# Performance work log

Measured on AMD Instinct MI355X. Metric: run time of the kernel, lower is better.

The kernel has to match this reference:

```python
import jax, jax.numpy as jnp
import numpy as np

B, S, I, H = 32, 512, 512, 512


def _lstm_dir(x_seq, Wih, Whh, bih, bhh, reverse):
    """Run a PyTorch-style LSTMCell over time. x_seq: [S, B, I]."""
    bsz = x_seq.shape[1]
    hid = Whh.shape[1]
    h0 = jnp.zeros((bsz, hid), x_seq.dtype)
    c0 = jnp.zeros((bsz, hid), x_seq.dtype)
    b = bih + bhh

    def step(carry, x_t):
        h, c = carry
        g = x_t @ Wih.T + h @ Whh.T + b           # [B, 4H]
        i_g, f_g, g_g, o_g = jnp.split(g, 4, axis=-1)
        c = jax.nn.sigmoid(f_g) * c + jax.nn.sigmoid(i_g) * jnp.tanh(g_g)
        h = jax.nn.sigmoid(o_g) * jnp.tanh(c)
        return (h, c), h

    (hN, cN), hs = jax.lax.scan(step, (h0, c0), x_seq, reverse=reverse)
    # with reverse=True, hs[t] is aligned with x_seq[t] (matches ht_b[::-1])
    return hs, hN, cN


def setup_inputs() -> dict:
    key = jax.random.key(0)
    ks = jax.random.split(key, 9)
    bound = 1.0 / np.sqrt(H)
    u = lambda k, shp: jax.random.uniform(k, shp, jnp.float32, -bound, bound)
    return {
        "X": jax.random.normal(ks[0], (B, S, I), jnp.float32),
        "Wih_f": u(ks[1], (4 * H, I)),
        "Whh_f": u(ks[2], (4 * H, H)),
        "bih_f": u(ks[3], (4 * H,)),
        "bhh_f": u(ks[4], (4 * H,)),
        "Wih_b": u(ks[5], (4 * H, I)),
        "Whh_b": u(ks[6], (4 * H, H)),
        "bih_b": u(ks[7], (4 * H,)),
        "bhh_b": u(ks[8], (4 * H,)),
    }


def reference(X, Wih_f, Whh_f, bih_f, bhh_f, Wih_b, Whh_b, bih_b, bhh_b):
    x_seq = jnp.transpose(X, (1, 0, 2))  # [S, B, I]
    hs_f, hN_f, cN_f = _lstm_dir(x_seq, Wih_f, Whh_f, bih_f, bhh_f, False)
    hs_b, hN_b, cN_b = _lstm_dir(x_seq, Wih_b, Whh_b, bih_b, bhh_b, True)
    # ht: [B, S, 2H]
    ht = jnp.transpose(jnp.concatenate([hs_f, hs_b], axis=-1), (1, 0, 2))
    stacked_h = jnp.stack([hN_f, hN_b])  # [2, B, H] (forward final, backward final)
    stacked_c = jnp.stack([cN_f, cN_b])
    return ht, (stacked_h, stacked_c)
```

## Files before the change

kernel.cpp:

```cpp
#include <hip/hip_runtime.h>
#include <hip/hip_bf16.h>

#define BSZ 32
#define SSZ 512
#define ISZ 512
#define HSZ 512
#define XB_OFF   0ull
#define HEX_OFF  (16ull << 20)
#define CTR_OFF  (HEX_OFF + (128ull << 10))

typedef __attribute__((ext_vector_type(8)))  short short8;
typedef __attribute__((ext_vector_type(4)))  float f32x4;
typedef __attribute__((ext_vector_type(4)))  unsigned short us4;
typedef __attribute__((ext_vector_type(4)))  int i32x4;

__device__ __forceinline__ unsigned short f2bf(float f) {
    union { float f; unsigned u; } v; v.f = f;
    unsigned r = v.u + 0x7fffu + ((v.u >> 16) & 1u);
    return (unsigned short)(r >> 16);
}

__device__ __forceinline__ float sigf(float x) { return 1.0f / (1.0f + __expf(-x)); }
__device__ __forceinline__ float tanhfast(float x) {
    float a = fabsf(x);
    float e = __expf(-2.0f * a);
    float t = (1.0f - e) / (1.0f + e);
    return x < 0.0f ? -t : t;
}

__global__ void k_xpose(const float* __restrict__ X, unsigned short* __restrict__ Xb) {
    int idx = blockIdx.x * 256 + threadIdx.x;
    int i4 = idx & 127;
    int t  = (idx >> 7) & 511;
    int b  = idx >> 16;
    float4 v = reinterpret_cast<const float4*>(X)[idx];
    us4 o = { f2bf(v.x), f2bf(v.y), f2bf(v.z), f2bf(v.w) };
    *reinterpret_cast<us4*>(Xb + (size_t)t * 16384 + (size_t)(i4 >> 1) * 256 + b * 8 + (i4 & 1) * 4) = o;
}

__launch_bounds__(256, 1)
__global__ void k_bilstm(const float* __restrict__ Wih_f, const float* __restrict__ Whh_f,
                         const float* __restrict__ bih_f, const float* __restrict__ bhh_f,
                         const float* __restrict__ Wih_b, const float* __restrict__ Whh_b,
                         const float* __restrict__ bih_b, const float* __restrict__ bhh_b,
                         const unsigned short* __restrict__ Xb,
                         unsigned short* h_ex, unsigned* flags, float* __restrict__ out)
{
    const int tid = threadIdx.x;
    const int grp = blockIdx.x & 7;
    if (grp >= 2) return;
    const int dir = grp;
    const int p   = blockIdx.x >> 3;
    const int wv  = tid >> 6;
    const int ln  = tid & 63;
    const int kh  = wv >> 1;
    const int sub = wv & 1;
    const int q   = ln >> 4;
    const int m15 = ln & 15;

    unsigned* tab = flags + 4096;
    {
        unsigned xcc;
        asm volatile("s_getreg_b32 %0, hwreg(20, 0, 32)" : "=s"(xcc));
        if (tid == 0)
            __hip_atomic_store(tab + dir * 32 + p, (xcc & 7u) + 1u,
                               __ATOMIC_RELAXED, __HIP_MEMORY_SCOPE_AGENT);
    }

    const float* Wih = dir ? Wih_b : Wih_f;
    const float* Whh = dir ? Whh_b : Whh_f;
    const float* bi  = dir ? bih_b : bih_f;
    const float* bh  = dir ? bhh_b : bhh_f;

    __shared__ float gates[3][32][67];
    __shared__ float cst[32][16];
    __shared__ float bias[64];
    __shared__ int   mode_sh;

    short8 breg[32];
    if (kh == 0) {
#pragma unroll
        for (int ks = 0; ks < 16; ++ks)
#pragma unroll
            for (int gg = 0; gg < 2; ++gg) {
                const float* wr = Wih + (size_t)((sub * 2 + gg) * 512 + p * 16 + m15) * 512
                                      + ks * 32 + q * 8;
                short8 bb;
#pragma unroll
                for (int j = 0; j < 8; ++j) bb[j] = (short)f2bf(wr[j]);
                breg[ks * 2 + gg] = bb;
            }
    } else {
#pragma unroll
        for (int ks = 0; ks < 8; ++ks)
#pragma unroll
            for (int g = 0; g < 4; ++g) {
                const float* wr = Whh + (size_t)(g * 512 + p * 16 + m15) * 512
                                      + sub * 256 + ks * 32 + q * 8;
                short8 bb;
#pragma unroll
                for (int j = 0; j < 8; ++j) bb[j] = (short)f2bf(wr[j]);
                breg[ks * 4 + g] = bb;
            }
    }

    if (tid < 64) {
        int c = tid;
        int gr = (c >> 4) * 512 + p * 16 + (c & 15);
        bias[c] = bi[gr] + bh[gr];
    }
    for (int i = tid; i < 512; i += 256) ((float*)cst)[i] = 0.0f;

    if (tid < 64) {
        const unsigned* tp = tab + dir * 32 + (tid & 31);
        unsigned v;
        do { v = __hip_atomic_load(tp, __ATOMIC_RELAXED, __HIP_MEMORY_SCOPE_AGENT); } while (v == 0u);
        unsigned ref = __shfl(v, 0);
        int same = (__ballot(v == ref) == ~0ull) ? 1 : 0;
        if (tid == 0) mode_sh = same;
    }
    __syncthreads();
    const int fast = mode_sh;

    unsigned* flg = flags + (size_t)dir * 2048;
    unsigned short* hexd = h_ex + (size_t)dir * 2 * 16384;

    int agent_poll = 0;

    for (int s = 0; s < 512; ++s) {
        const int t = dir ? (511 - s) : s;
        f32x4 acc[4][2];
#pragma unroll
        for (int g = 0; g < 4; ++g) { acc[g][0] = {0.f,0.f,0.f,0.f}; acc[g][1] = {0.f,0.f,0.f,0.f}; }

        if (kh == 0) {
            const unsigned short* abase = Xb + (size_t)t * 16384;
#pragma unroll
            for (int ks = 0; ks < 16; ++ks) {
                const unsigned short* ap = abase + (size_t)(ks * 4 + q) * 256 + m15 * 8;
                short8 a0 = *reinterpret_cast<const short8*>(ap);
                short8 a1 = *reinterpret_cast<const short8*>(ap + 128);
                acc[0][0] = __builtin_amdgcn_mfma_f32_16x16x32_bf16(a0, breg[ks * 2 + 0], acc[0][0], 0, 0, 0);
                acc[1][0] = __builtin_amdgcn_mfma_f32_16x16x32_bf16(a0, breg[ks * 2 + 1], acc[1][0], 0, 0, 0);
                acc[0][1] = __builtin_amdgcn_mfma_f32_16x16x32_bf16(a1, breg[ks * 2 + 0], acc[0][1], 0, 0, 0);
                acc[1][1] = __builtin_amdgcn_mfma_f32_16x16x32_bf16(a1, breg[ks * 2 + 1], acc[1][1], 0, 0, 0);
            }
#pragma unroll
            for (int gg = 0; gg < 2; ++gg)
#pragma unroll
                for (int r = 0; r < 4; ++r) {
                    gates[0][q * 4 + r][(sub * 2 + gg) * 16 + m15]      = acc[gg][0][r];
                    gates[0][16 + q * 4 + r][(sub * 2 + gg) * 16 + m15] = acc[gg][1][r];
                }
        } else if (fast) {
            if (s > 0) {
                const unsigned* fp = flg + (ln & 31);
                if (!agent_poll) {
                    int spins = 0;
                    for (;;) {
                        unsigned v;
                        asm volatile("global_load_dword %0, %1, off sc0\n\t"
                                     "s_waitcnt vmcnt(0)"
                                     : "=&v"(v) : "v"(fp) : "memory");
                        if (__ballot((int)(v >= (unsigned)s)) == ~0ull) break;
                        if (++spins > 20000) { agent_poll = 1; break; }
                    }
                }
                if (agent_poll) {
                    for (;;) {
                        unsigned v = __hip_atomic_load(fp, __ATOMIC_RELAXED, __HIP_MEMORY_SCOPE_AGENT);
                        if (__ballot((int)(v >= (unsigned)s)) == ~0ull) break;
                    }
                }
                asm volatile("" ::: "memory");
            }
            const unsigned short* ab = hexd + (size_t)((s + 1) & 1) * 16384 + sub * 8192;
            i32x4 A0[8], A1[8];
#pragma unroll
            for (int ks = 0; ks < 8; ++ks) {
                const unsigned short* ap = ab + (size_t)(ks * 4 + q) * 256 + m15 * 8;
                asm volatile("global_load_dwordx4 %0, %2, off sc0\n\t"
                             "global_load_dwordx4 %1, %3, off sc0"
                             : "=&v"(A0[ks]), "=&v"(A1[ks])
                             : "v"(ap), "v"(ap + 128) : "memory");
            }
#pragma unroll
            for (int ks = 0; ks < 8; ++ks) {
                asm volatile("s_waitcnt vmcnt(%0)" :: "n"(14 - 2 * ks) : "memory");
                __builtin_amdgcn_sched_barrier(0);
                short8 a0 = __builtin_bit_cast(short8, A0[ks]);
                short8 a1 = __builtin_bit_cast(short8, A1[ks]);
#pragma unroll
                for (int g = 0; g < 4; ++g) {
                    acc[g][0] = __builtin_amdgcn_mfma_f32_16x16x32_bf16(a0, breg[ks * 4 + g], acc[g][0], 0, 0, 0);
                    acc[g][1] = __builtin_amdgcn_mfma_f32_16x16x32_bf16(a1, breg[ks * 4 + g], acc[g][1], 0, 0, 0);
                }
            }
#pragma unroll
            for (int g = 0; g < 4; ++g)
#pragma unroll
                for (int r = 0; r < 4; ++r) {
                    gates[1 + sub][q * 4 + r][g * 16 + m15]      = acc[g][0][r];
                    gates[1 + sub][16 + q * 4 + r][g * 16 + m15] = acc[g][1][r];
                }
        } else {
            if (s > 0) {
                const unsigned* fp = flg + (ln & 31);
                for (;;) {
                    unsigned v = __hip_atomic_load(fp, __ATOMIC_RELAXED, __HIP_MEMORY_SCOPE_AGENT);
                    if (__ballot((int)(v >= (unsigned)s)) == ~0ull) break;
                }
                asm volatile("" ::: "memory");
            }
            const unsigned* abase = reinterpret_cast<const unsigned*>(
                hexd + (size_t)((s + 1) & 1) * 16384 + sub * 8192);
#pragma unroll
            for (int ks = 0; ks < 8; ++ks) {
                const unsigned* ap = abase + ((ks * 4 + q) * 256 + m15 * 8) / 2;
                union { short8 s8; unsigned u[4]; } ua0, ua1;
#pragma unroll
                for (int w = 0; w < 4; ++w) {
                    ua0.u[w] = __hip_atomic_load(ap + w,      __ATOMIC_RELAXED, __HIP_MEMORY_SCOPE_AGENT);
                    ua1.u[w] = __hip_atomic_load(ap + 64 + w, __ATOMIC_RELAXED, __HIP_MEMORY_SCOPE_AGENT);
                }
#pragma unroll
                for (int g = 0; g < 4; ++g) {
                    acc[g][0] = __builtin_amdgcn_mfma_f32_16x16x32_bf16(ua0.s8, breg[ks * 4 + g], acc[g][0], 0, 0, 0);
                    acc[g][1] = __builtin_amdgcn_mfma_f32_16x16x32_bf16(ua1.s8, breg[ks * 4 + g], acc[g][1], 0, 0, 0);
                }
            }
#pragma unroll
            for (int g = 0; g < 4; ++g)
#pragma unroll
                for (int r = 0; r < 4; ++r) {
                    gates[1 + sub][q * 4 + r][g * 16 + m15]      = acc[g][0][r];
                    gates[1 + sub][16 + q * 4 + r][g * 16 + m15] = acc[g][1][r];
                }
        }

        __syncthreads();

        int b  = tid >> 3;
        int j0 = (tid & 7) * 2;
        float hv01[2], cn01[2];
        {
#pragma unroll
            for (int u = 0; u < 2; ++u) {
                int j = j0 + u;
                float ig = gates[0][b][j]      + gates[1][b][j]      + gates[2][b][j]      + bias[j];
                float fg = gates[0][b][16 + j] + gates[1][b][16 + j] + gates[2][b][16 + j] + bias[16 + j];
                float gg = gates[0][b][32 + j] + gates[1][b][32 + j] + gates[2][b][32 + j] + bias[32 + j];
                float og = gates[0][b][48 + j] + gates[1][b][48 + j] + gates[2][b][48 + j] + bias[48 + j];
                float cn = sigf(fg) * cst[b][j] + sigf(ig) * tanhfast(gg);
                cst[b][j] = cn;
                float hv = sigf(og) * tanhfast(cn);
                hv01[u] = hv; cn01[u] = cn;
            }
            int hc0 = p * 16 + j0;
            unsigned pk = (unsigned)f2bf(hv01[0]) | ((unsigned)f2bf(hv01[1]) << 16);
            unsigned* dst = reinterpret_cast<unsigned*>(
                hexd + (size_t)(s & 1) * 16384 + (size_t)(hc0 >> 3) * 256 + b * 8 + (hc0 & 7));
            if (fast) {
                asm volatile("global_store_dword %0, %1, off sc0" :: "v"(dst), "v"(pk) : "memory");
            } else {
                __hip_atomic_store(dst, pk, __ATOMIC_RELAXED, __HIP_MEMORY_SCOPE_AGENT);
            }
        }

        asm volatile("s_waitcnt vmcnt(0)" ::: "memory");
        __syncthreads();
        if (tid == 0) {
            if (fast) {
                unsigned sv = (unsigned)(s + 1);
                asm volatile("global_store_dword %0, %1, off sc0" :: "v"(flg + p), "v"(sv) : "memory");
            } else {
                __hip_atomic_store(flg + p, (unsigned)(s + 1), __ATOMIC_RELAXED, __HIP_MEMORY_SCOPE_AGENT);
            }
        }

#pragma unroll
        for (int u = 0; u < 2; ++u) {
            int hc = p * 16 + j0 + u;
            out[(size_t)b * (512 * 1024) + (size_t)t * 1024 + dir * 512 + hc] = hv01[u];
            if (s == 511) {
                out[16777216 + dir * 16384 + b * 512 + hc] = hv01[u];
                out[16777216 + 32768 + dir * 16384 + b * 512 + hc] = cn01[u];
            }
        }
    }
}

extern "C" void kernel_launch(void* const* d_in, const int* in_sizes, int n_in,
                              void* d_out, int out_size, void* d_ws, size_t ws_size,
                              hipStream_t stream) {
    const float* X     = (const float*)d_in[0];
    const float* Wih_f = (const float*)d_in[1];
    const float* Whh_f = (const float*)d_in[2];
    const float* bih_f = (const float*)d_in[3];
    const float* bhh_f = (const float*)d_in[4];
    const float* Wih_b = (const float*)d_in[5];
    const float* Whh_b = (const float*)d_in[6];
    const float* bih_b = (const float*)d_in[7];
    const float* bhh_b = (const float*)d_in[8];
    float* out = (float*)d_out;

    unsigned short* Xb   = (unsigned short*)((char*)d_ws + XB_OFF);
    unsigned short* h_ex = (unsigned short*)((char*)d_ws + HEX_OFF);
    unsigned*       flg  = (unsigned*)((char*)d_ws + CTR_OFF);

    hipMemsetAsync((char*)d_ws + HEX_OFF, 0, (128ull + 64ull) << 10, stream);
    k_xpose<<<8192, 256, 0, stream>>>(X, Xb);
    k_bilstm<<<256, 256, 0, stream>>>(Wih_f, Whh_f, bih_f, bhh_f,
                                      Wih_b, Whh_b, bih_b, bhh_b,
                                      Xb, h_ex, flg, out);
}
```

Measured before the change: 2.496 ms.

## Double-buffer gate scratch and use per-wave flags to drop per-step barrier

The shared gate buffer is double-buffered by step parity, which lets the second __syncthreads after the cell update be removed. Completion is now signalled per wave instead of per block: each wave's lane 0 writes its own flag slot, and consumers poll 128 flags (two loads per lane) instead of 32. This targets the intra-block barrier on the serial recurrence critical path. The cost is doubled LDS use for gates and wider flag polling traffic, and it relies on per-wave ordering of the h stores before the flag store.

```diff
diff --git a/kernel.cpp b/kernel.cpp
--- a/kernel.cpp
+++ b/kernel.cpp
@@ -72,7 +72,7 @@
     const float* bi  = dir ? bih_b : bih_f;
     const float* bh  = dir ? bhh_b : bhh_f;
 
-    __shared__ float gates[3][32][67];
+    __shared__ float gates[2][3][32][67];
     __shared__ float cst[32][16];
     __shared__ float bias[64];
     __shared__ int   mode_sh;
@@ -132,6 +132,8 @@
         f32x4 acc[4][2];
 #pragma unroll
         for (int g = 0; g < 4; ++g) { acc[g][0] = {0.f,0.f,0.f,0.f}; acc[g][1] = {0.f,0.f,0.f,0.f}; }
+
+        float (*gw)[32][67] = gates[s & 1];
 
         if (kh == 0) {
             const unsigned short* abase = Xb + (size_t)t * 16384;
@@ -149,27 +151,30 @@
             for (int gg = 0; gg < 2; ++gg)
 #pragma unroll
                 for (int r = 0; r < 4; ++r) {
-                    gates[0][q * 4 + r][(sub * 2 + gg) * 16 + m15]      = acc[gg][0][r];
-                    gates[0][16 + q * 4 + r][(sub * 2 + gg) * 16 + m15] = acc[gg][1][r];
+                    gw[0][q * 4 + r][(sub * 2 + gg) * 16 + m15]      = acc[gg][0][r];
+                    gw[0][16 + q * 4 + r][(sub * 2 + gg) * 16 + m15] = acc[gg][1][r];
                 }
         } else if (fast) {
             if (s > 0) {
-                const unsigned* fp = flg + (ln & 31);
+                const unsigned* fp0 = flg + ln;
+                const unsigned* fp1 = flg + 64 + ln;
                 if (!agent_poll) {
                     int spins = 0;
                     for (;;) {
-                        unsigned v;
-                        asm volatile("global_load_dword %0, %1, off sc0\n\t"
+                        unsigned v0, v1;
+                        asm volatile("global_load_dword %0, %2, off sc0\n\t"
+                                     "global_load_dword %1, %3, off sc0\n\t"
                                      "s_waitcnt vmcnt(0)"
-                                     : "=&v"(v) : "v"(fp) : "memory");
-                        if (__ballot((int)(v >= (unsigned)s)) == ~0ull) break;
+                                     : "=&v"(v0), "=&v"(v1) : "v"(fp0), "v"(fp1) : "memory");
+                        if (__ballot((int)(v0 >= (unsigned)s) & (int)(v1 >= (unsigned)s)) == ~0ull) break;
                         if (++spins > 20000) { agent_poll = 1; break; }
                     }
                 }
                 if (agent_poll) {
                     for (;;) {
-                        unsigned v = __hip_atomic_load(fp, __ATOMIC_RELAXED, __HIP_MEMORY_SCOPE_AGENT);
-                        if (__ballot((int)(v >= (unsigned)s)) == ~0ull) break;
+                        unsigned v0 = __hip_atomic_load(fp0, __ATOMIC_RELAXED, __HIP_MEMORY_SCOPE_AGENT);
+                        unsigned v1 = __hip_atomic_load(fp1, __ATOMIC_RELAXED, __HIP_MEMORY_SCOPE_AGENT);
+                        if (__ballot((int)(v0 >= (unsigned)s) & (int)(v1 >= (unsigned)s)) == ~0ull) break;
                     }
                 }
                 asm volatile("" ::: "memory");
@@ -200,15 +205,17 @@
             for (int g = 0; g < 4; ++g)
 #pragma unroll
                 for (int r = 0; r < 4; ++r) {
-                    gates[1 + sub][q * 4 + r][g * 16 + m15]      = acc[g][0][r];
-                    gates[1 + sub][16 + q * 4 + r][g * 16 + m15] = acc[g][1][r];
+                    gw[1 + sub][q * 4 + r][g * 16 + m15]      = acc[g][0][r];
+                    gw[1 + sub][16 + q * 4 + r][g * 16 + m15] = acc[g][1][r];
                 }
         } else {
             if (s > 0) {
-                const unsigned* fp = flg + (ln & 31);
+                const unsigned* fp0 = flg + ln;
+                const unsigned* fp1 = flg + 64 + ln;
                 for (;;) {
-                    unsigned v = __hip_atomic_load(fp, __ATOMIC_RELAXED, __HIP_MEMORY_SCOPE_AGENT);
-                    if (__ballot((int)(v >= (unsigned)s)) == ~0ull) break;
+                    unsigned v0 = __hip_atomic_load(fp0, __ATOMIC_RELAXED, __HIP_MEMORY_SCOPE_AGENT);
+                    unsigned v1 = __hip_atomic_load(fp1, __ATOMIC_RELAXED, __HIP_MEMORY_SCOPE_AGENT);
+                    if (__ballot((int)(v0 >= (unsigned)s) & (int)(v1 >= (unsigned)s)) == ~0ull) break;
                 }
                 asm volatile("" ::: "memory");
             }
@@ -233,8 +240,8 @@
             for (int g = 0; g < 4; ++g)
 #pragma unroll
                 for (int r = 0; r < 4; ++r) {
-                    gates[1 + sub][q * 4 + r][g * 16 + m15]      = acc[g][0][r];
-                    gates[1 + sub][16 + q * 4 + r][g * 16 + m15] = acc[g][1][r];
+                    gw[1 + sub][q * 4 + r][g * 16 + m15]      = acc[g][0][r];
+                    gw[1 + sub][16 + q * 4 + r][g * 16 + m15] = acc[g][1][r];
                 }
         }
 
@@ -247,10 +254,10 @@
 #pragma unroll
             for (int u = 0; u < 2; ++u) {
                 int j = j0 + u;
-                float ig = gates[0][b][j]      + gates[1][b][j]      + gates[2][b][j]      + bias[j];
-                float fg = gates[0][b][16 + j] + gates[1][b][16 + j] + gates[2][b][16 + j] + bias[16 + j];
-                float gg = gates[0][b][32 + j] + gates[1][b][32 + j] + gates[2][b][32 + j] + bias[32 + j];
-                float og = gates[0][b][48 + j] + gates[1][b][48 + j] + gates[2][b][48 + j] + bias[48 + j];
+                float ig = gw[0][b][j]      + gw[1][b][j]      + gw[2][b][j]      + bias[j];
+                float fg = gw[0][b][16 + j] + gw[1][b][16 + j] + gw[2][b][16 + j] + bias[16 + j];
+                float gg = gw[0][b][32 + j] + gw[1][b][32 + j] + gw[2][b][32 + j] + bias[32 + j];
+                float og = gw[0][b][48 + j] + gw[1][b][48 + j] + gw[2][b][48 + j] + bias[48 + j];
                 float cn = sigf(fg) * cst[b][j] + sigf(ig) * tanhfast(gg);
                 cst[b][j] = cn;
                 float hv = sigf(og) * tanhfast(cn);
@@ -268,13 +275,13 @@
         }
 
         asm volatile("s_waitcnt vmcnt(0)" ::: "memory");
-        __syncthreads();
-        if (tid == 0) {
+        if (ln == 0) {
+            unsigned sv = (unsigned)(s + 1);
+            unsigned* fdst = flg + (p * 4 + wv);
             if (fast) {
-                unsigned sv = (unsigned)(s + 1);
-                asm volatile("global_store_dword %0, %1, off sc0" :: "v"(flg + p), "v"(sv) : "memory");
+                asm volatile("global_store_dword %0, %1, off sc0" :: "v"(fdst), "v"(sv) : "memory");
             } else {
-                __hip_atomic_store(flg + p, (unsigned)(s + 1), __ATOMIC_RELAXED, __HIP_MEMORY_SCOPE_AGENT);
+                __hip_atomic_store(fdst, sv, __ATOMIC_RELAXED, __HIP_MEMORY_SCOPE_AGENT);
             }
         }
 
```

Measured after the change: 4.263 ms. 1.71x slower.
